# Performance work log

Measured on AMD Instinct MI355X. Metric: run time of the kernel, lower is better.

The kernel has to match this reference:

```python
import jax, jax.numpy as jnp
import numpy as np

D_MODEL = 1024
NHEAD = 16
HEAD_DIM = D_MODEL // NHEAD


def setup_inputs() -> dict:
    key = jax.random.key(0)
    k_x, k_wqkv, k_bqkv, k_wo, k_bo = jax.random.split(key, 5)
    scale_in = 1.0 / np.sqrt(D_MODEL)
    x = jax.random.normal(k_x, (2, 2048, D_MODEL), dtype=jnp.float32)
    # qkv_proj: Linear(d_model, 3*d_model); stored as [in, out] for x @ W
    W_qkv = jax.random.uniform(k_wqkv, (D_MODEL, 3 * D_MODEL), dtype=jnp.float32,
                               minval=-scale_in, maxval=scale_in)
    b_qkv = jax.random.uniform(k_bqkv, (3 * D_MODEL,), dtype=jnp.float32,
                               minval=-scale_in, maxval=scale_in)
    W_out = jax.random.uniform(k_wo, (D_MODEL, D_MODEL), dtype=jnp.float32,
                               minval=-scale_in, maxval=scale_in)
    b_out = jax.random.uniform(k_bo, (D_MODEL,), dtype=jnp.float32,
                               minval=-scale_in, maxval=scale_in)
    return {"x": x, "W_qkv": W_qkv, "b_qkv": b_qkv, "W_out": W_out, "b_out": b_out}


def reference(x, W_qkv, b_qkv, W_out, b_out):
    B, S, _ = x.shape
    qkv = x @ W_qkv + b_qkv                                   # [B,S,3*d_model]
    # Faithful to torch module: reshape to [B,S,H,3*hd], move heads, chunk LAST dim
    qkv = qkv.reshape(B, S, NHEAD, 3 * HEAD_DIM)
    qkv = qkv.transpose(0, 2, 1, 3)                            # [B,H,S,3*hd]
    q, k, v = jnp.split(qkv, 3, axis=-1)                       # each [B,H,S,hd]
    scale = 1.0 / np.sqrt(HEAD_DIM).astype(np.float32)
    attn = jnp.einsum('bhqd,bhkd->bhqk', q, k) * scale         # [B,H,S,S]
    attn = jax.nn.softmax(attn, axis=-1)
    out = jnp.einsum('bhqk,bhkd->bhqd', attn, v)               # [B,H,S,hd]
    out = out.transpose(0, 2, 1, 3).reshape(B, S, D_MODEL)     # [B,S,d_model]
    return out @ W_out + b_out
```

## Files before the change

### kernel.cpp

```cpp
#include <hip/hip_runtime.h>
#include <cmath>

typedef unsigned short u16;
typedef unsigned int u32;
typedef __bf16 bf16x8 __attribute__((ext_vector_type(8)));
typedef float f32x4 __attribute__((ext_vector_type(4)));

#define D_MODEL 1024
#define NHEAD 16
#define HD 64
#define SEQ 2048
#define BATCH 2
#define M_TOK 4096
#define N_QKV 3072

#define LOG2E 1.4426950408889634f
#define SOFTMAX_SHIFT 11.541560327111707f

__device__ __forceinline__ u16 f2bf(float f) {
    u32 u = __float_as_uint(f);
    u32 r = (u + 0x7fffu + ((u >> 16) & 1u)) >> 16;
    return (u16)r;
}

__device__ __forceinline__ float bf2f(u16 v) {
    return __uint_as_float(((u32)v) << 16);
}

__device__ __forceinline__ u32 pack_bf(float a, float b) {
    u32 ua = __float_as_uint(a) + 0x8000u;
    u32 ub = __float_as_uint(b) + 0x8000u;
    return __builtin_amdgcn_perm(ub, ua, 0x07060302u);
}

__device__ __forceinline__ bf16x8 ld_bf8(const u16* p) {
    return *(const bf16x8*)p;
}

__device__ __forceinline__ bf16x8 as_bf8(int4 v) {
    union { int4 i; bf16x8 b; } u; u.i = v; return u.b;
}

__device__ __forceinline__ f32x4 mfma16(bf16x8 a, bf16x8 b, f32x4 c) {
    return __builtin_amdgcn_mfma_f32_16x16x32_bf16(a, b, c, 0, 0, 0);
}

__device__ __forceinline__ void gload_lds16(const u16* g, u16* l) {
    __builtin_amdgcn_global_load_lds(
        (const __attribute__((address_space(1))) void*)g,
        (__attribute__((address_space(3))) void*)l, 16, 0, 0);
}

__global__ void cast_x_kernel(const float* __restrict__ in, u16* __restrict__ out, int n4) {
    int i = blockIdx.x * blockDim.x + threadIdx.x;
    int stride = gridDim.x * blockDim.x;
    for (; i < n4; i += stride) {
        float4 v = ((const float4*)in)[i];
        ushort4 o;
        o.x = f2bf(v.x); o.y = f2bf(v.y); o.z = f2bf(v.z); o.w = f2bf(v.w);
        ((ushort4*)out)[i] = o;
    }
}

template <int ROWS, int COLS>
__global__ void transpose_cast_kernel(const float* __restrict__ in, u16* __restrict__ out) {
    __shared__ float tile[32][33];
    int c0 = blockIdx.x * 32;
    int r0 = blockIdx.y * 32;
    int tx = threadIdx.x;
    int ty = threadIdx.y;
#pragma unroll
    for (int i = 0; i < 32; i += 8)
        tile[ty + i][tx] = in[(size_t)(r0 + ty + i) * COLS + c0 + tx];
    __syncthreads();
#pragma unroll
    for (int i = 0; i < 32; i += 8)
        out[(size_t)(c0 + ty + i) * ROWS + r0 + tx] = f2bf(tile[tx][ty + i]);
}

__global__ __launch_bounds__(256) void gemm_qkv_kernel(
    const u16* __restrict__ A, const u16* __restrict__ Bt, const float* __restrict__ bias,
    u16* __restrict__ Qb, u16* __restrict__ Kb, u16* __restrict__ Vp)
{
    __shared__ u16 lA[128 * 32];
    __shared__ u16 lB[128 * 32];
    int w = threadIdx.x >> 6, l = threadIdx.x & 63;
    int col = l & 15, quad = l >> 4;
    int wm = w >> 1, wn = w & 1;
    int m0 = blockIdx.x * 128;
    int n0 = blockIdx.y * 128;
    int lrow = l >> 2;
    int lcol = (l & 3) * 8;

    f32x4 acc[4][4] = {};
    for (int k0 = 0; k0 < 1024; k0 += 32) {
        __syncthreads();
#pragma unroll
        for (int i = 0; i < 2; i++) {
            int slab = w * 32 + i * 16;
            gload_lds16(A  + (size_t)(m0 + slab + lrow) * 1024 + k0 + lcol, lA + slab * 32);
            gload_lds16(Bt + (size_t)(n0 + slab + lrow) * 1024 + k0 + lcol, lB + slab * 32);
        }
        __syncthreads();
        bf16x8 af[4], bfr[4];
#pragma unroll
        for (int i = 0; i < 4; i++)
            af[i] = ld_bf8(lA + (wm * 64 + i * 16 + col) * 32 + quad * 8);
#pragma unroll
        for (int j = 0; j < 4; j++)
            bfr[j] = ld_bf8(lB + (wn * 64 + j * 16 + col) * 32 + quad * 8);
#pragma unroll
        for (int i = 0; i < 4; i++)
#pragma unroll
            for (int j = 0; j < 4; j++)
                acc[i][j] = mfma16(af[i], bfr[j], acc[i][j]);
    }

#pragma unroll
    for (int i = 0; i < 4; i++) {
#pragma unroll
        for (int j = 0; j < 4; j++) {
            int cc = n0 + wn * 64 + j * 16 + col;
            int h = cc / 192;
            int within = cc - h * 192;
            int ww = within >> 6;
            int d = within & 63;
            float bv = bias[cc];
#pragma unroll
            for (int r = 0; r < 4; r++) {
                int row = m0 + wm * 64 + i * 16 + quad * 4 + r;
                int b = row >> 11;
                int s = row & 2047;
                int bh = b * NHEAD + h;
                float val = acc[i][j][r] + bv;
                if (ww == 0)     Qb[(size_t)(bh * SEQ + s) * HD + d] = f2bf(val * 0.125f);
                else if (ww == 1) Kb[(size_t)(bh * SEQ + s) * HD + d] = f2bf(val);
                else {
                    int sp = (s & ~31) | ((s & 12) << 1) | (((s >> 4) & 1) << 2) | (s & 3);
                    Vp[(size_t)(bh * HD + d) * SEQ + sp] = f2bf(val);
                }
            }
        }
    }
}

__global__ __launch_bounds__(256, 4) void attn_kernel(
    const u16* __restrict__ Qb, const u16* __restrict__ Kb,
    const u16* __restrict__ Vp, u16* __restrict__ O0,
    u16* __restrict__ O1, float* __restrict__ Lp)
{
    __shared__ u16 kbuf[2][64 * 64];
    __shared__ u16 vbuf[2][64 * 64];
    int wave = threadIdx.x >> 6, lane = threadIdx.x & 63;
    int col = lane & 15, quad = lane >> 4;
    int g = blockIdx.x;
    int xcd = g & 7, slot = g >> 3;
    int bh = xcd * 4 + (slot >> 5);
    int rem = slot & 31;
    int split = rem >> 4;
    int qt = rem & 15;
    int q0 = qt * 128 + wave * 32;
    int kstart = split * 16;

    int srow = lane >> 3;
    int sgrp = (lane & 7) ^ srow;
    const u16* Kt0 = Kb + (size_t)bh * SEQ * HD;
    const u16* Vt0 = Vp + (size_t)bh * HD * SEQ;
    long soffK = (long)srow * HD + sgrp * 8;
    long soffV = (long)srow * SEQ + sgrp * 8;
    int r0 = wave * 16;

    int rbase = col * 64;
    int sw0 = ((quad)     ^ (col & 7)) * 8;
    int sw1 = ((quad + 4) ^ (col & 7)) * 8;

    bf16x8 aq[2][2];
#pragma unroll
    for (int m = 0; m < 2; m++) {
        const u16* qbase = Qb + ((size_t)bh * SEQ + q0 + m * 16 + col) * HD + quad * 8;
        aq[m][0] = ld_bf8(qbase);
        aq[m][1] = ld_bf8(qbase + 32);
    }

    f32x4 o[2][4] = {};
    float lsum[2] = {0.f, 0.f};

    {
        int kbase = kstart * 64;
        gload_lds16(Kt0 + (size_t)(kbase + r0) * HD + soffK,     kbuf[0] + r0 * 64);
        gload_lds16(Kt0 + (size_t)(kbase + r0 + 8) * HD + soffK, kbuf[0] + (r0 + 8) * 64);
        gload_lds16(Vt0 + (size_t)r0 * SEQ + kbase + soffV,      vbuf[0] + r0 * 64);
        gload_lds16(Vt0 + (size_t)(r0 + 8) * SEQ + kbase + soffV, vbuf[0] + (r0 + 8) * 64);
    }

    for (int kt = 0; kt < 16; ++kt) {
        int cur = kt & 1;
        __syncthreads();
        if (kt + 1 < 16) {
            int kbase = (kstart + kt + 1) * 64;
            int nb = cur ^ 1;
            gload_lds16(Kt0 + (size_t)(kbase + r0) * HD + soffK,     kbuf[nb] + r0 * 64);
            gload_lds16(Kt0 + (size_t)(kbase + r0 + 8) * HD + soffK, kbuf[nb] + (r0 + 8) * 64);
            gload_lds16(Vt0 + (size_t)r0 * SEQ + kbase + soffV,      vbuf[nb] + r0 * 64);
            gload_lds16(Vt0 + (size_t)(r0 + 8) * SEQ + kbase + soffV, vbuf[nb] + (r0 + 8) * 64);
        }
        const u16* kb = kbuf[cur];
        const u16* vb = vbuf[cur];
        bf16x8 kf[4][2];
#pragma unroll
        for (int t = 0; t < 4; t++) {
            kf[t][0] = ld_bf8(kb + t * 1024 + rbase + sw0);
            kf[t][1] = ld_bf8(kb + t * 1024 + rbase + sw1);
        }
        int4 vraw[4][2];
#pragma unroll
        for (int t = 0; t < 4; t++) {
            vraw[t][0] = *(const int4*)(vb + t * 1024 + rbase + sw0);
            vraw[t][1] = *(const int4*)(vb + t * 1024 + rbase + sw1);
        }
        int4 pfrag[2][2];
#pragma unroll
        for (int m = 0; m < 2; m++) {
#pragma unroll
            for (int t = 0; t < 4; t++) {
                f32x4 sa = {};
                sa = mfma16(kf[t][0], aq[m][0], sa);
                sa = mfma16(kf[t][1], aq[m][1], sa);
                f32x4 p;
#pragma unroll
                for (int r = 0; r < 4; r++)
                    p[r] = __builtin_exp2f(__builtin_fmaf(sa[r], LOG2E, -SOFTMAX_SHIFT));
                lsum[m] += (p[0] + p[1]) + (p[2] + p[3]);
                u32 lo = pack_bf(p[0], p[1]);
                u32 hi = pack_bf(p[2], p[3]);
                if ((t & 1) == 0) { pfrag[m][t >> 1].x = (int)lo; pfrag[m][t >> 1].y = (int)hi; }
                else              { pfrag[m][t >> 1].z = (int)lo; pfrag[m][t >> 1].w = (int)hi; }
            }
        }
#pragma unroll
        for (int m = 0; m < 2; m++)
#pragma unroll
            for (int t = 0; t < 4; t++)
#pragma unroll
                for (int h = 0; h < 2; h++)
                    o[m][t] = mfma16(as_bf8(pfrag[m][h]), as_bf8(vraw[t][h]), o[m][t]);
    }

    u16* Op = split ? O1 : O0;
#pragma unroll
    for (int m = 0; m < 2; m++) {
        float lr = lsum[m];
        lr += __shfl_xor(lr, 16);
        lr += __shfl_xor(lr, 32);
        if (quad == 0)
            Lp[(size_t)split * 32 * SEQ + (size_t)bh * SEQ + q0 + m * 16 + col] = lr;
#pragma unroll
        for (int r = 0; r < 4; r++) {
            int srow2 = q0 + m * 16 + quad * 4 + r;
#pragma unroll
            for (int t = 0; t < 4; t++)
                Op[((size_t)bh * SEQ + srow2) * HD + t * 16 + col] = f2bf(o[m][t][r]);
        }
    }
}

__global__ __launch_bounds__(256) void combine_kernel(
    const u16* __restrict__ O0, const u16* __restrict__ O1,
    const float* __restrict__ Lp, u16* __restrict__ At)
{
    int i = blockIdx.x * 256 + threadIdx.x;
    int dg = i & 15;
    int q = (i >> 4) & 2047;
    int bh = i >> 15;
    size_t ob = ((size_t)bh * SEQ + q) * HD + dg * 4;
    ushort4 a = *(const ushort4*)(O0 + ob);
    ushort4 b = *(const ushort4*)(O1 + ob);
    float l = Lp[(size_t)bh * SEQ + q] + Lp[(size_t)32 * SEQ + (size_t)bh * SEQ + q];
    float inv = 1.f / l;
    int bb = bh >> 4, h = bh & 15;
    ushort4 o;
    o.x = f2bf((bf2f(a.x) + bf2f(b.x)) * inv);
    o.y = f2bf((bf2f(a.y) + bf2f(b.y)) * inv);
    o.z = f2bf((bf2f(a.z) + bf2f(b.z)) * inv);
    o.w = f2bf((bf2f(a.w) + bf2f(b.w)) * inv);
    *(ushort4*)(At + ((size_t)(bb * SEQ + q)) * D_MODEL + h * 64 + dg * 4) = o;
}

__global__ __launch_bounds__(256) void gemm_out_kernel(
    const u16* __restrict__ A, const u16* __restrict__ Bt, const float* __restrict__ bias,
    float* __restrict__ out)
{
    __shared__ u16 lA[128 * 32];
    __shared__ u16 lB[128 * 32];
    int w = threadIdx.x >> 6, l = threadIdx.x & 63;
    int col = l & 15, quad = l >> 4;
    int wm = w >> 1, wn = w & 1;
    int m0 = blockIdx.x * 128;
    int n0 = blockIdx.y * 128;
    int lrow = l >> 2;
    int lcol = (l & 3) * 8;

    f32x4 acc[4][4] = {};
    for (int k0 = 0; k0 < 1024; k0 += 32) {
        __syncthreads();
#pragma unroll
        for (int i = 0; i < 2; i++) {
            int slab = w * 32 + i * 16;
            gload_lds16(A  + (size_t)(m0 + slab + lrow) * 1024 + k0 + lcol, lA + slab * 32);
            gload_lds16(Bt + (size_t)(n0 + slab + lrow) * 1024 + k0 + lcol, lB + slab * 32);
        }
        __syncthreads();
        bf16x8 af[4], bfr[4];
#pragma unroll
        for (int i = 0; i < 4; i++)
            af[i] = ld_bf8(lA + (wm * 64 + i * 16 + col) * 32 + quad * 8);
#pragma unroll
        for (int j = 0; j < 4; j++)
            bfr[j] = ld_bf8(lB + (wn * 64 + j * 16 + col) * 32 + quad * 8);
#pragma unroll
        for (int i = 0; i < 4; i++)
#pragma unroll
            for (int j = 0; j < 4; j++)
                acc[i][j] = mfma16(af[i], bfr[j], acc[i][j]);
    }

#pragma unroll
    for (int i = 0; i < 4; i++) {
#pragma unroll
        for (int j = 0; j < 4; j++) {
            int cc = n0 + wn * 64 + j * 16 + col;
            float bv = bias[cc];
#pragma unroll
            for (int r = 0; r < 4; r++) {
                int row = m0 + wm * 64 + i * 16 + quad * 4 + r;
                out[(size_t)row * D_MODEL + cc] = acc[i][j][r] + bv;
            }
        }
    }
}

extern "C" void kernel_launch(void* const* d_in, const int* in_sizes, int n_in,
                              void* d_out, int out_size, void* d_ws, size_t ws_size,
                              hipStream_t stream) {
    const float* x     = (const float*)d_in[0];
    const float* W_qkv = (const float*)d_in[1];
    const float* b_qkv = (const float*)d_in[2];
    const float* W_out = (const float*)d_in[3];
    const float* b_out = (const float*)d_in[4];
    float* out = (float*)d_out;

    char* ws = (char*)d_ws;
    u16* Xb    = (u16*)(ws);
    u16* Wqkvt = (u16*)(ws + (8ull << 20));
    u16* Qb    = (u16*)(ws + (16ull << 20));
    u16* Kb    = (u16*)(ws + (24ull << 20));
    u16* Vp    = (u16*)(ws + (32ull << 20));
    u16* O0    = (u16*)(ws);
    u16* O1    = (u16*)(ws + (8ull << 20));
    float* Lp  = (float*)(ws + (40ull << 20));
    u16* At    = (u16*)(ws + (16ull << 20));
    u16* Woutt = (u16*)(ws);

    cast_x_kernel<<<1024, 256, 0, stream>>>(x, Xb, M_TOK * D_MODEL / 4);
    transpose_cast_kernel<1024, 3072><<<dim3(96, 32), dim3(32, 8), 0, stream>>>(W_qkv, Wqkvt);
    gemm_qkv_kernel<<<dim3(32, 24), 256, 0, stream>>>(Xb, Wqkvt, b_qkv, Qb, Kb, Vp);
    attn_kernel<<<dim3(1024), 256, 0, stream>>>(Qb, Kb, Vp, O0, O1, Lp);
    combine_kernel<<<dim3(BATCH * NHEAD * SEQ * (HD / 4) / 256), 256, 0, stream>>>(O0, O1, Lp, At);
    transpose_cast_kernel<1024, 1024><<<dim3(32, 32), dim3(32, 8), 0, stream>>>(W_out, Woutt);
    gemm_out_kernel<<<dim3(32, 8), 256, 0, stream>>>(At, Woutt, b_out, out);
}
```

Before: 212.8 us.

## Stage V tile in LDS for coalesced stores, compute row sums via MFMA

The QKV GEMM epilogue now writes the permuted V values into a shared-memory tile and then stores them to global memory as contiguous 16-byte vectors, replacing scattered 2-byte transposed writes. The attention kernel computes softmax row sums with an extra MFMA against a vector of ones, using the bf16-rounded probabilities, instead of scalar adds plus cross-lane shuffles. pack_bf uses the hardware packed bf16 convert when that builtin is available. The cost is extra LDS and a barrier in the GEMM, two more MFMAs per tile, and a row sum taken from bf16-rounded values.

```diff
diff --git a/kernel.cpp b/kernel.cpp
--- a/kernel.cpp
+++ b/kernel.cpp
@@ -28,9 +28,16 @@
 }
 
 __device__ __forceinline__ u32 pack_bf(float a, float b) {
+#if __has_builtin(__builtin_amdgcn_cvt_pk_bf16_f32)
+    typedef __bf16 bf16x2_t __attribute__((ext_vector_type(2)));
+    union { bf16x2_t v; u32 u; } c;
+    c.v = __builtin_amdgcn_cvt_pk_bf16_f32(a, b);
+    return c.u;
+#else
     u32 ua = __float_as_uint(a) + 0x8000u;
     u32 ub = __float_as_uint(b) + 0x8000u;
     return __builtin_amdgcn_perm(ub, ua, 0x07060302u);
+#endif
 }
 
 __device__ __forceinline__ bf16x8 ld_bf8(const u16* p) {
@@ -49,6 +56,12 @@
     __builtin_amdgcn_global_load_lds(
         (const __attribute__((address_space(1))) void*)g,
         (__attribute__((address_space(3))) void*)l, 16, 0, 0);
+}
+
+__device__ __forceinline__ int Gv(int x) {
+    int q = x / 192, rm = x - q * 192;
+    int e = rm - 128;
+    return q * 64 + (e > 0 ? e : 0);
 }
 
 __global__ void cast_x_kernel(const float* __restrict__ in, u16* __restrict__ out, int n4) {
@@ -84,6 +97,7 @@
 {
     __shared__ u16 lA[128 * 32];
     __shared__ u16 lB[128 * 32];
+    __shared__ u16 vtile[64 * 132];
     int w = threadIdx.x >> 6, l = threadIdx.x & 63;
     int col = l & 15, quad = l >> 4;
     int wm = w >> 1, wn = w & 1;
@@ -116,6 +130,8 @@
                 acc[i][j] = mfma16(af[i], bfr[j], acc[i][j]);
     }
 
+    int s0 = m0 & 2047;
+    int bblk = m0 >> 11;
 #pragma unroll
     for (int i = 0; i < 4; i++) {
 #pragma unroll
@@ -125,22 +141,33 @@
             int within = cc - h * 192;
             int ww = within >> 6;
             int d = within & 63;
+            int vloc = Gv(cc) - Gv(n0);
             float bv = bias[cc];
 #pragma unroll
             for (int r = 0; r < 4; r++) {
-                int row = m0 + wm * 64 + i * 16 + quad * 4 + r;
-                int b = row >> 11;
-                int s = row & 2047;
-                int bh = b * NHEAD + h;
+                int sloc = wm * 64 + i * 16 + quad * 4 + r;
+                int s = s0 + sloc;
+                int bh = bblk * NHEAD + h;
                 float val = acc[i][j][r] + bv;
-                if (ww == 0)     Qb[(size_t)(bh * SEQ + s) * HD + d] = f2bf(val * 0.125f);
+                if (ww == 0)      Qb[(size_t)(bh * SEQ + s) * HD + d] = f2bf(val * 0.125f);
                 else if (ww == 1) Kb[(size_t)(bh * SEQ + s) * HD + d] = f2bf(val);
                 else {
-                    int sp = (s & ~31) | ((s & 12) << 1) | (((s >> 4) & 1) << 2) | (s & 3);
-                    Vp[(size_t)(bh * HD + d) * SEQ + sp] = f2bf(val);
+                    int sp = (sloc & ~31) | ((sloc & 12) << 1) | (((sloc >> 4) & 1) << 2) | (sloc & 3);
+                    vtile[vloc * 132 + sp] = f2bf(val);
                 }
             }
         }
+    }
+    __syncthreads();
+    int vcols = Gv(n0 + 128) - Gv(n0);
+    int gbase = Gv(n0);
+    for (int c = threadIdx.x; c < vcols * 16; c += 256) {
+        int vloc = c >> 4, gi = c & 15;
+        int av = gbase + vloc;
+        int h = av >> 6, d = av & 63;
+        int bh = bblk * NHEAD + h;
+        int4 vv = *(const int4*)(vtile + vloc * 132 + gi * 8);
+        *(int4*)(Vp + ((size_t)(bh * HD + d)) * SEQ + s0 + gi * 8) = vv;
     }
 }
 
@@ -174,6 +201,10 @@
     int sw0 = ((quad)     ^ (col & 7)) * 8;
     int sw1 = ((quad + 4) ^ (col & 7)) * 8;
 
+    union { u32 w[4]; int4 i; } onesu;
+    onesu.w[0] = onesu.w[1] = onesu.w[2] = onesu.w[3] = 0x3F803F80u;
+    bf16x8 ones = as_bf8(onesu.i);
+
     bf16x8 aq[2][2];
 #pragma unroll
     for (int m = 0; m < 2; m++) {
@@ -183,13 +214,13 @@
     }
 
     f32x4 o[2][4] = {};
-    float lsum[2] = {0.f, 0.f};
+    f32x4 ol[2] = {};
 
     {
         int kbase = kstart * 64;
-        gload_lds16(Kt0 + (size_t)(kbase + r0) * HD + soffK,     kbuf[0] + r0 * 64);
-        gload_lds16(Kt0 + (size_t)(kbase + r0 + 8) * HD + soffK, kbuf[0] + (r0 + 8) * 64);
-        gload_lds16(Vt0 + (size_t)r0 * SEQ + kbase + soffV,      vbuf[0] + r0 * 64);
+        gload_lds16(Kt0 + (size_t)(kbase + r0) * HD + soffK,      kbuf[0] + r0 * 64);
+        gload_lds16(Kt0 + (size_t)(kbase + r0 + 8) * HD + soffK,  kbuf[0] + (r0 + 8) * 64);
+        gload_lds16(Vt0 + (size_t)r0 * SEQ + kbase + soffV,       vbuf[0] + r0 * 64);
         gload_lds16(Vt0 + (size_t)(r0 + 8) * SEQ + kbase + soffV, vbuf[0] + (r0 + 8) * 64);
     }
 
@@ -199,9 +230,9 @@
         if (kt + 1 < 16) {
             int kbase = (kstart + kt + 1) * 64;
             int nb = cur ^ 1;
-            gload_lds16(Kt0 + (size_t)(kbase + r0) * HD + soffK,     kbuf[nb] + r0 * 64);
-            gload_lds16(Kt0 + (size_t)(kbase + r0 + 8) * HD + soffK, kbuf[nb] + (r0 + 8) * 64);
-            gload_lds16(Vt0 + (size_t)r0 * SEQ + kbase + soffV,      vbuf[nb] + r0 * 64);
+            gload_lds16(Kt0 + (size_t)(kbase + r0) * HD + soffK,      kbuf[nb] + r0 * 64);
+            gload_lds16(Kt0 + (size_t)(kbase + r0 + 8) * HD + soffK,  kbuf[nb] + (r0 + 8) * 64);
+            gload_lds16(Vt0 + (size_t)r0 * SEQ + kbase + soffV,       vbuf[nb] + r0 * 64);
             gload_lds16(Vt0 + (size_t)(r0 + 8) * SEQ + kbase + soffV, vbuf[nb] + (r0 + 8) * 64);
         }
         const u16* kb = kbuf[cur];
@@ -230,7 +261,6 @@
 #pragma unroll
                 for (int r = 0; r < 4; r++)
                     p[r] = __builtin_exp2f(__builtin_fmaf(sa[r], LOG2E, -SOFTMAX_SHIFT));
-                lsum[m] += (p[0] + p[1]) + (p[2] + p[3]);
                 u32 lo = pack_bf(p[0], p[1]);
                 u32 hi = pack_bf(p[2], p[3]);
                 if ((t & 1) == 0) { pfrag[m][t >> 1].x = (int)lo; pfrag[m][t >> 1].y = (int)hi; }
@@ -238,25 +268,25 @@
             }
         }
 #pragma unroll
-        for (int m = 0; m < 2; m++)
+        for (int m = 0; m < 2; m++) {
 #pragma unroll
             for (int t = 0; t < 4; t++)
 #pragma unroll
                 for (int h = 0; h < 2; h++)
                     o[m][t] = mfma16(as_bf8(pfrag[m][h]), as_bf8(vraw[t][h]), o[m][t]);
+            ol[m] = mfma16(as_bf8(pfrag[m][0]), ones, ol[m]);
+            ol[m] = mfma16(as_bf8(pfrag[m][1]), ones, ol[m]);
+        }
     }
 
     u16* Op = split ? O1 : O0;
 #pragma unroll
     for (int m = 0; m < 2; m++) {
-        float lr = lsum[m];
-        lr += __shfl_xor(lr, 16);
-        lr += __shfl_xor(lr, 32);
-        if (quad == 0)
-            Lp[(size_t)split * 32 * SEQ + (size_t)bh * SEQ + q0 + m * 16 + col] = lr;
 #pragma unroll
         for (int r = 0; r < 4; r++) {
             int srow2 = q0 + m * 16 + quad * 4 + r;
+            if (col == 0)
+                Lp[(size_t)split * 32 * SEQ + (size_t)bh * SEQ + srow2] = ol[m][r];
 #pragma unroll
             for (int t = 0; t < 4; t++)
                 Op[((size_t)bh * SEQ + srow2) * HD + t * 16 + col] = f2bf(o[m][t][r]);
```

Measured after the change: 208.5 us. -2.0%, faster.
